# Optimization experiments

Measured on AMD Instinct MI355X. Metric: run time of the kernel, lower is better.

Reference implementation:

```python
import jax, jax.numpy as jnp
import numpy as np

M_MAX = 8
GN_GROUPS = 8  # _pick_gn_groups(64)
HEADS = 4
G_C = 19
PER_C = 16


def silu(x):
    return x * jax.nn.sigmoid(x)


def layer_norm(x, g, b, eps=1e-5):
    mu = x.mean(-1, keepdims=True)
    var = ((x - mu) ** 2).mean(-1, keepdims=True)
    return (x - mu) * jax.lax.rsqrt(var + eps) * g + b


def group_norm(x, g, b, eps=1e-5):
    N, C, H, W = x.shape
    xr = x.reshape(N, GN_GROUPS, C // GN_GROUPS, H, W)
    mu = xr.mean((2, 3, 4), keepdims=True)
    var = ((xr - mu) ** 2).mean((2, 3, 4), keepdims=True)
    xn = ((xr - mu) * jax.lax.rsqrt(var + eps)).reshape(N, C, H, W)
    return xn * g[:, None, None] + b[:, None, None]


def conv1x1(x, w):  # x [N,C,H,W], w [O,C]
    return jnp.einsum('nchw,oc->nohw', x, w)


def dw3x3(x, w):  # depthwise 3x3, w [C,1,3,3]
    return jax.lax.conv_general_dilated(x, w, (1, 1), 'SAME', feature_group_count=x.shape[1], dimension_numbers=('NCHW', 'OIHW', 'NCHW'))


def forward(board, stem_w, stem_g, stem_b, qw, qb, kw, kb, vw, vb, ow, ob, ln_g, ln_b, dw_w, gn1_g, gn1_b, pw_w, gn2_g, gn2_b, pol_w, pol_b, vh_w1, vh_b1, vh_w2, vh_b2, om_w, om_b, op_w1, op_b1, op_w2, op_b2):
    B, Cin, H, W = board.shape
    hid = stem_w.shape[0]
    hd = hid // HEADS
    g = board[:, :G_C]
    p = board[:, G_C:G_C + M_MAX * PER_C].reshape(B, M_MAX, PER_C, H, W)
    player_in = jnp.concatenate([jnp.broadcast_to(g[:, None], (B, M_MAX, G_C, H, W)), p], axis=2)
    x = conv1x1(player_in.reshape(B * M_MAX, G_C + PER_C, H, W), stem_w)
    x = silu(group_norm(x, stem_g, stem_b)).reshape(B, M_MAX, hid, H, W)
    m_each = jnp.argmax(board[:, 7:14, 0, 0], axis=1) + 2  # number of players in [2,8]
    present = jnp.arange(M_MAX) < m_each[:, None]  # [B, M_MAX] bool
    neg = jnp.finfo(board.dtype).min
    L = qw.shape[0]
    for i in range(L):
        tokens = x.transpose(0, 3, 4, 1, 2).reshape(B, H * W, M_MAX, hid)
        q = (tokens @ qw[i].T + qb[i]).reshape(B, H * W, M_MAX, HEADS, hd)
        k = (tokens @ kw[i].T + kb[i]).reshape(B, H * W, M_MAX, HEADS, hd)
        v = (tokens @ vw[i].T + vb[i]).reshape(B, H * W, M_MAX, HEADS, hd)
        logits = jnp.einsum('bnqhd,bnkhd->bnhqk', q, k) * (hd ** -0.5)
        logits = jnp.where(present[:, None, None, None, :], logits, neg)
        attn = jax.nn.softmax(logits, axis=-1)
        ao = jnp.einsum('bnhqk,bnkhd->bnqhd', attn, v).reshape(B, H * W, M_MAX, hid)
        tokens = layer_norm(tokens + ao @ ow[i].T + ob[i], ln_g[i], ln_b[i])
        xc = tokens.reshape(B, H, W, M_MAX, hid).transpose(0, 3, 4, 1, 2).reshape(B * M_MAX, hid, H, W)
        y = silu(group_norm(dw3x3(xc, dw_w[i]), gn1_g[i], gn1_b[i]))
        y = group_norm(conv1x1(y, pw_w[i]), gn2_g[i], gn2_b[i])
        xc = silu(xc + y)
        x = xc.reshape(B, M_MAX, hid, H, W) * present[:, :, None, None, None].astype(xc.dtype)
    x0 = x[:, 0]
    logits_p = (conv1x1(x0, pol_w) + pol_b[:, None, None]).reshape(B, H * W)
    pooled0 = x0.mean((2, 3))
    value = (silu(pooled0 @ vh_w1.T + vh_b1) @ vh_w2.T + vh_b2)[:, 0]
    move_all = (conv1x1(x.reshape(B * M_MAX, hid, H, W), om_w) + om_b[:, None, None]).reshape(B, M_MAX, M_MAX, H * W)
    pooled_all = x.mean((3, 4))
    param_all = (silu(pooled_all @ op_w1.T + op_b1) @ op_w2.T + op_b2).reshape(B, M_MAX, M_MAX, 5)
    idx = jnp.arange(M_MAX)
    pf = present[..., None]
    opp_move = move_all[:, idx, idx, :] * pf.astype(move_all.dtype)
    opp_param = param_all[:, idx, idx, :] * pf.astype(param_all.dtype)
    return (logits_p, value, opp_move, opp_param)


def setup_inputs() -> dict:
    key = jax.random.key(0)
    ks = iter(jax.random.split(key, 48))
    def rn(shape, s=0.1):
        return jax.random.normal(next(ks), shape, jnp.float32) * s
    B, H, W, C, L = 16, 32, 32, 64, 6
    inp = {
        'board': jax.random.normal(next(ks), (B, 149, H, W), jnp.float32),
        'stem_w': rn((C, 35)), 'stem_g': jnp.ones((C,)), 'stem_b': jnp.zeros((C,)),
        'qw': rn((L, C, C)), 'qb': rn((L, C), 0.01),
        'kw': rn((L, C, C)), 'kb': rn((L, C), 0.01),
        'vw': rn((L, C, C)), 'vb': rn((L, C), 0.01),
        'ow': rn((L, C, C)), 'ob': rn((L, C), 0.01),
        'ln_g': jnp.ones((L, C)), 'ln_b': jnp.zeros((L, C)),
        'dw_w': rn((L, C, 1, 3, 3)),
        'gn1_g': jnp.ones((L, C)), 'gn1_b': jnp.zeros((L, C)),
        'pw_w': rn((L, C, C)),
        'gn2_g': jnp.ones((L, C)), 'gn2_b': jnp.zeros((L, C)),
        'pol_w': rn((1, C)), 'pol_b': jnp.zeros((1,)),
        'vh_w1': rn((C, C)), 'vh_b1': jnp.zeros((C,)),
        'vh_w2': rn((1, C)), 'vh_b2': jnp.zeros((1,)),
        'om_w': rn((M_MAX, C)), 'om_b': jnp.zeros((M_MAX,)),
        'op_w1': rn((C, C)), 'op_b1': jnp.zeros((C,)),
        'op_w2': rn((M_MAX * 5, C)), 'op_b2': jnp.zeros((M_MAX * 5,)),
    }
    return inp


def reference(board, stem_w, stem_g, stem_b, qw, qb, kw, kb, vw, vb, ow, ob, ln_g, ln_b, dw_w, gn1_g, gn1_b, pw_w, gn2_g, gn2_b, pol_w, pol_b, vh_w1, vh_b1, vh_w2, vh_b2, om_w, om_b, op_w1, op_b1, op_w2, op_b2):
    return forward(board, stem_w, stem_g, stem_b, qw, qb, kw, kb, vw, vb, ow, ob, ln_g, ln_b, dw_w, gn1_g, gn1_b, pw_w, gn2_g, gn2_b, pol_w, pol_b, vh_w1, vh_b1, vh_w2, vh_b2, om_w, om_b, op_w1, op_b1, op_w2, op_b2)
```

## Files before the change

kernel.cpp:

```cpp
#include <hip/hip_runtime.h>
#include <cstddef>


#define WSX   0u
#define WST   8388608u
#define WSY   16777216u
#define WSS   25165824u
#define WSP   (WSS + 26624u)
#define WSPL  (WSP + 128u)

#define ATTN_LDS_BYTES ((4 * 64 * 64 + 8 * 64 * 8) * 4)

__device__ __forceinline__ float silu_f(float x) { return x / (1.f + __expf(-x)); }

__device__ __forceinline__ float wsum64(float v) {
#pragma unroll
  for (int s = 1; s < 64; s <<= 1) v += __shfl_xor(v, s);
  return v;
}

__device__ __forceinline__ float rowsum16(float v) {
  v += __int_as_float(__builtin_amdgcn_update_dpp(0, __float_as_int(v), 0x128, 0xf, 0xf, true));
  v += __int_as_float(__builtin_amdgcn_update_dpp(0, __float_as_int(v), 0x124, 0xf, 0xf, true));
  v += __int_as_float(__builtin_amdgcn_update_dpp(0, __float_as_int(v), 0x122, 0xf, 0xf, true));
  v += __int_as_float(__builtin_amdgcn_update_dpp(0, __float_as_int(v), 0x121, 0xf, 0xf, true));
  return v;
}

__device__ __forceinline__ float wsum64b(float v) {
  v = rowsum16(v);
  v += __shfl_xor(v, 16);
  v += __shfl_xor(v, 32);
  return v;
}

__global__ __launch_bounds__(256) void k_init(const float* __restrict__ board,
                                              float* __restrict__ ws) {
  int tid = threadIdx.x;
  for (unsigned i = blockIdx.x * 256 + tid; i < 26624u; i += 64u * 256u) ws[WSS + i] = 0.f;
  if (blockIdx.x == 0 && tid < 128) {
    int b = tid >> 3, m = tid & 7;
    float best = board[(size_t)(b * 149 + 7) * 1024];
    int bi = 0;
    for (int ch = 1; ch < 7; ++ch) {
      float v = board[(size_t)(b * 149 + 7 + ch) * 1024];
      if (v > best) { best = v; bi = ch; }
    }
    int m_each = bi + 2;
    ws[WSP + tid] = (m < m_each) ? 1.f : 0.f;
  }
}

__global__ __launch_bounds__(256) void k_stem(const float* __restrict__ board,
                                              const float* __restrict__ stem_w,
                                              float* __restrict__ ws) {
  __shared__ float A[147 * 64];
  __shared__ float WT[35 * 64];
  __shared__ float red_s[256], red_ss[256];
  int tid = threadIdx.x;
  int b = blockIdx.x >> 4, n0 = (blockIdx.x & 15) * 64;
  for (int i = tid; i < 147 * 64; i += 256) {
    int c = i >> 6, p = i & 63;
    A[i] = board[(size_t)(b * 149 + c) * 1024 + n0 + p];
  }
  for (int i = tid; i < 35 * 64; i += 256) {
    int o = i / 35, c = i % 35;
    WT[c * 64 + o] = stem_w[i];
  }
  __syncthreads();
  int o = tid & 63, wv = tid >> 6;
  float* X = ws + WSX;
  float st_s[8], st_ss[8];
#pragma unroll
  for (int m = 0; m < 8; ++m) { st_s[m] = 0.f; st_ss[m] = 0.f; }
  for (int m = 0; m < 8; ++m) {
    for (int k = 0; k < 4; ++k) {
      int q = wv + 4 * k;
      float a0 = 0.f, a1 = 0.f, a2 = 0.f, a3 = 0.f;
#pragma unroll
      for (int c = 0; c < 19; ++c) {
        float w = WT[c * 64 + o];
        float4 av = *(const float4*)&A[c * 64 + q * 4];
        a0 += av.x * w; a1 += av.y * w; a2 += av.z * w; a3 += av.w * w;
      }
#pragma unroll
      for (int j = 0; j < 16; ++j) {
        float w = WT[(19 + j) * 64 + o];
        float4 av = *(const float4*)&A[(19 + m * 16 + j) * 64 + q * 4];
        a0 += av.x * w; a1 += av.y * w; a2 += av.z * w; a3 += av.w * w;
      }
      int n = n0 + q * 4;
      float vals[4] = {a0, a1, a2, a3};
#pragma unroll
      for (int j = 0; j < 4; ++j) {
        X[((size_t)(b * 1024 + n + j) * 8 + m) * 64 + o] = vals[j];
        st_s[m] += vals[j];
        st_ss[m] += vals[j] * vals[j];
      }
    }
  }
  float* stats = ws + WSS;
  for (int m = 0; m < 8; ++m) {
    __syncthreads();
    red_s[tid] = st_s[m];
    red_ss[tid] = st_ss[m];
    __syncthreads();
    if (tid < 8) {
      float a = 0.f, a2 = 0.f;
      for (int w4 = 0; w4 < 4; ++w4)
        for (int j = 0; j < 8; ++j) {
          int t2 = w4 * 64 + tid * 8 + j;
          a += red_s[t2]; a2 += red_ss[t2];
        }
      atomicAdd(&stats[((b * 8 + m) * 8 + tid) * 2 + 0], a);
      atomicAdd(&stats[((b * 8 + m) * 8 + tid) * 2 + 1], a2);
    }
  }
}

__global__ __launch_bounds__(256) void k_gn_silu(float* __restrict__ X,
                                                 const float* __restrict__ g,
                                                 const float* __restrict__ bt,
                                                 const float* __restrict__ stats) {
  for (size_t idx = (size_t)blockIdx.x * 256 + threadIdx.x; idx < 8388608ull;
       idx += (size_t)2048 * 256) {
    int c = (int)(idx & 63);
    int m = (int)((idx >> 6) & 7);
    int b = (int)(idx >> 19);
    int gi = ((b * 8 + m) * 8 + (c >> 3)) * 2;
    float s = stats[gi], s2 = stats[gi + 1];
    float mean = s * (1.f / 8192.f);
    float var = s2 * (1.f / 8192.f) - mean * mean;
    float rstd = rsqrtf(var + 1e-5f);
    float v = (X[idx] - mean) * rstd * g[c] + bt[c];
    X[idx] = silu_f(v);
  }
}

#define FMA8(acc, WW)                                                      \
  acc[0] += t0.x * (WW); acc[1] += t0.y * (WW); acc[2] += t0.z * (WW);     \
  acc[3] += t0.w * (WW); acc[4] += t1.x * (WW); acc[5] += t1.y * (WW);     \
  acc[6] += t1.z * (WW); acc[7] += t1.w * (WW);

__global__ __launch_bounds__(512, 4) void k_attn(
    const float* __restrict__ Xin, const float* __restrict__ Yin,
    const float* __restrict__ s2p, const float* __restrict__ g2p,
    const float* __restrict__ b2p, float* __restrict__ T,
    const float* __restrict__ qw, const float* __restrict__ qb,
    const float* __restrict__ kw, const float* __restrict__ kb,
    const float* __restrict__ vw, const float* __restrict__ vb,
    const float* __restrict__ ow, const float* __restrict__ ob,
    const float* __restrict__ lng, const float* __restrict__ lnb,
    const float* __restrict__ present, int fused) {
  extern __shared__ float sm[];
  float* Wq = sm;
  float* Wk = sm + 4096;
  float* Wv = sm + 8192;
  float* Wo = sm + 12288;
  float* BUF = sm + 16384;
  int tid = threadIdx.x;
  int lane = tid & 63, wv = tid >> 6;
  int b = blockIdx.x >> 5;
  int n0 = (blockIdx.x & 31) * 32;
  for (int i = tid; i < 4096; i += 512) {
    int o = i >> 6, c = i & 63;
    Wq[c * 64 + o] = qw[i];
    Wk[c * 64 + o] = kw[i];
    Wv[c * 64 + o] = vw[i];
    Wo[c * 64 + o] = ow[i];
  }
  float bq = qb[lane], bk = kb[lane], bv = vb[lane], bo = ob[lane];
  float gl = lng[lane], bl = lnb[lane];
  unsigned pmask = 0;
#pragma unroll
  for (int m = 0; m < 8; ++m) pmask |= (present[b * 8 + m] > 0.5f) ? (1u << m) : 0u;
  float Ag[8], Bg[8];
  if (fused) {
    int g = lane >> 3;
    float gw = g2p[lane], bw_ = b2p[lane];
#pragma unroll
    for (int m = 0; m < 8; ++m) {
      int gi = ((b * 8 + m) * 8 + g) * 2;
      float sg = s2p[gi], sg2 = s2p[gi + 1];
      float mean = sg * (1.f / 8192.f);
      float var = sg2 * (1.f / 8192.f) - mean * mean;
      float rstd = rsqrtf(var + 1e-5f);
      Ag[m] = rstd * gw;
      Bg[m] = bw_ - mean * Ag[m];
    }
  }
  __syncthreads();
  float* bw = BUF + wv * 512;
  const int sw = lane & 12;
  for (int j = 0; j < 4; ++j) {
    int n = n0 + wv * 4 + j;
    size_t pbase = ((size_t)(b * 1024 + n) * 8) * 64 + lane;
    float tok[8];
    if (fused) {
#pragma unroll
      for (int m = 0; m < 8; ++m) {
        float tv = Xin[pbase + m * 64];
        float yv = Yin[pbase + m * 64];
        float z = tv + (yv * Ag[m] + Bg[m]);
        float pres = ((pmask >> m) & 1) ? 1.f : 0.f;
        tok[m] = silu_f(z) * pres;
      }
    } else {
#pragma unroll
      for (int m = 0; m < 8; ++m) tok[m] = Xin[pbase + m * 64];
    }
    *(float4*)&bw[(lane * 8) ^ sw]     = make_float4(tok[0], tok[1], tok[2], tok[3]);
    *(float4*)&bw[(lane * 8 + 4) ^ sw] = make_float4(tok[4], tok[5], tok[6], tok[7]);
    __asm__ volatile("" ::: "memory");
    float aq[8], ak[8], av[8];
#pragma unroll
    for (int m = 0; m < 8; ++m) { aq[m] = bq; ak[m] = bk; av[m] = bv; }
#pragma unroll
    for (int c = 0; c < 64; ++c) {
      float4 t0 = *(const float4*)&bw[(c * 8) ^ (c & 12)];
      float4 t1 = *(const float4*)&bw[(c * 8 + 4) ^ (c & 12)];
      float wq_ = Wq[c * 64 + lane];
      float wk_ = Wk[c * 64 + lane];
      float wv_ = Wv[c * 64 + lane];
      FMA8(aq, wq_)
      FMA8(ak, wk_)
      FMA8(av, wv_)
    }
    float ao[8];
#pragma unroll
    for (int mq = 0; mq < 8; ++mq) {
      float lg[8];
#pragma unroll
      for (int mk = 0; mk < 8; ++mk)
        lg[mk] = rowsum16(aq[mq] * ak[mk]) * 0.25f;
      float mx = -3.0e38f;
#pragma unroll
      for (int mk = 0; mk < 8; ++mk)
        if ((pmask >> mk) & 1) mx = fmaxf(mx, lg[mk]);
      float se = 0.f, acc = 0.f;
#pragma unroll
      for (int mk = 0; mk < 8; ++mk) {
        float e = ((pmask >> mk) & 1) ? __expf(lg[mk] - mx) : 0.f;
        se += e;
        acc += e * av[mk];
      }
      ao[mq] = acc * __builtin_amdgcn_rcpf(se);
    }
    __asm__ volatile("" ::: "memory");
    *(float4*)&bw[(lane * 8) ^ sw]     = make_float4(ao[0], ao[1], ao[2], ao[3]);
    *(float4*)&bw[(lane * 8 + 4) ^ sw] = make_float4(ao[4], ao[5], ao[6], ao[7]);
    __asm__ volatile("" ::: "memory");
    float z[8];
#pragma unroll
    for (int m = 0; m < 8; ++m) z[m] = bo;
#pragma unroll
    for (int c = 0; c < 64; ++c) {
      float4 t0 = *(const float4*)&bw[(c * 8) ^ (c & 12)];
      float4 t1 = *(const float4*)&bw[(c * 8 + 4) ^ (c & 12)];
      float wo_ = Wo[c * 64 + lane];
      FMA8(z, wo_)
    }
    __asm__ volatile("" ::: "memory");
    float* tp = T + pbase;
#pragma unroll
    for (int m = 0; m < 8; ++m) {
      float r = tok[m] + z[m];
      float mean = wsum64b(r) * (1.f / 64.f);
      float d = r - mean;
      float var = wsum64b(d * d) * (1.f / 64.f);
      float rstd = rsqrtf(var + 1e-5f);
      tp[m * 64] = d * rstd * gl + bl;
    }
  }
}

__global__ __launch_bounds__(256) void k_dw(const float* __restrict__ T, float* __restrict__ Y,
                                            const float* __restrict__ dww,
                                            float* __restrict__ stats) {
  __shared__ float red_s[256], red_ss[256];
  int tid = threadIdx.x;
  int b = blockIdx.x >> 5, r = blockIdx.x & 31;
  int half = tid >> 7;
  int mc4 = tid & 127;
  int m = mc4 >> 4, c4 = mc4 & 15, c0 = c4 * 4;
  float4 w9[9];
#pragma unroll
  for (int t = 0; t < 9; ++t) {
    w9[t].x = dww[(c0 + 0) * 9 + t];
    w9[t].y = dww[(c0 + 1) * 9 + t];
    w9[t].z = dww[(c0 + 2) * 9 + t];
    w9[t].w = dww[(c0 + 3) * 9 + t];
  }
  float s = 0.f, ss = 0.f;
  const size_t plane = (size_t)b * 524288 + (size_t)m * 64 + c0;
  for (int ci = 0; ci < 16; ++ci) {
    int col = half * 16 + ci;
    float4 acc = make_float4(0.f, 0.f, 0.f, 0.f);
#pragma unroll
    for (int dh = -1; dh <= 1; ++dh) {
      int rr = r + dh;
      if (rr < 0 || rr > 31) continue;
#pragma unroll
      for (int dx = -1; dx <= 1; ++dx) {
        int cc = col + dx;
        if (cc < 0 || cc > 31) continue;
        float4 tv = *(const float4*)&T[plane + (size_t)(rr * 32 + cc) * 512];
        float4 w = w9[(dh + 1) * 3 + dx + 1];
        acc.x += tv.x * w.x; acc.y += tv.y * w.y;
        acc.z += tv.z * w.z; acc.w += tv.w * w.w;
      }
    }
    *(float4*)&Y[plane + (size_t)(r * 32 + col) * 512] = acc;
    s += acc.x + acc.y + acc.z + acc.w;
    ss += acc.x * acc.x + acc.y * acc.y + acc.z * acc.z + acc.w * acc.w;
  }
  red_s[tid] = s;
  red_ss[tid] = ss;
  __syncthreads();
  if (tid < 64) {
    int mm = tid >> 3, g = tid & 7;
    float a = 0.f, a2 = 0.f;
#pragma unroll
    for (int hh = 0; hh < 2; ++hh)
#pragma unroll
      for (int e = 0; e < 2; ++e) {
        int idx = hh * 128 + mm * 16 + g * 2 + e;
        a += red_s[idx];
        a2 += red_ss[idx];
      }
    atomicAdd(&stats[((b * 8 + mm) * 8 + g) * 2 + 0], a);
    atomicAdd(&stats[((b * 8 + mm) * 8 + g) * 2 + 1], a2);
  }
}

__global__ __launch_bounds__(256) void k_pw(float* __restrict__ Y, const float* __restrict__ pw,
                                            const float* __restrict__ g1,
                                            const float* __restrict__ b1,
                                            const float* __restrict__ s1,
                                            float* __restrict__ s2) {
  __shared__ float PWT[4096];
  __shared__ float HB[4][256];
  __shared__ float red_s[256], red_ss[256];
  int tid = threadIdx.x, lane = tid & 63, wv = tid >> 6;
  int bm = blockIdx.x >> 2, pt = blockIdx.x & 3;
  int b = bm >> 3, m = bm & 7;
  int n0 = pt * 256;
  for (int i = tid; i < 4096; i += 256) {
    int o = i >> 6, c = i & 63;
    PWT[c * 64 + o] = pw[i];
  }
  int g = lane >> 3;
  float sg = s1[(bm * 8 + g) * 2], sg2 = s1[(bm * 8 + g) * 2 + 1];
  float mean = sg * (1.f / 8192.f);
  float var = sg2 * (1.f / 8192.f) - mean * mean;
  float rstd = rsqrtf(var + 1e-5f);
  float A = rstd * g1[lane];
  float Bc = b1[lane] - mean * A;
  __syncthreads();
  float st = 0.f, st2 = 0.f;
  const size_t base = (size_t)b * 1024 * 512 + (size_t)m * 64 + lane;
  for (int it = 0; it < 16; ++it) {
    int n = n0 + it * 16 + wv * 4;
    float h[4];
#pragma unroll
    for (int jj = 0; jj < 4; ++jj) {
      float y = Y[base + (size_t)(n + jj) * 512];
      h[jj] = silu_f(y * A + Bc);
    }
    *(float4*)&HB[wv][lane * 4] = make_float4(h[0], h[1], h[2], h[3]);
    __asm__ volatile("" ::: "memory");
    float a0 = 0.f, a1 = 0.f, a2 = 0.f, a3 = 0.f;
#pragma unroll 8
    for (int c = 0; c < 64; ++c) {
      float4 hh = *(const float4*)&HB[wv][c * 4];
      float w = PWT[c * 64 + lane];
      a0 += hh.x * w; a1 += hh.y * w; a2 += hh.z * w; a3 += hh.w * w;
    }
    float vals[4] = {a0, a1, a2, a3};
#pragma unroll
    for (int jj = 0; jj < 4; ++jj) {
      Y[base + (size_t)(n + jj) * 512] = vals[jj];
      st += vals[jj];
      st2 += vals[jj] * vals[jj];
    }
    __asm__ volatile("" ::: "memory");
  }
  red_s[tid] = st;
  red_ss[tid] = st2;
  __syncthreads();
  if (tid < 8) {
    float a = 0.f, a2 = 0.f;
    for (int w4 = 0; w4 < 4; ++w4)
      for (int j = 0; j < 8; ++j) {
        int t2 = w4 * 64 + tid * 8 + j;
        a += red_s[t2]; a2 += red_ss[t2];
      }
    atomicAdd(&s2[(bm * 8 + tid) * 2 + 0], a);
    atomicAdd(&s2[(bm * 8 + tid) * 2 + 1], a2);
  }
}

__global__ __launch_bounds__(256) void k_fuse(const float* __restrict__ T,
                                              const float* __restrict__ Y,
                                              float* __restrict__ X,
                                              const float* __restrict__ g2,
                                              const float* __restrict__ b2,
                                              const float* __restrict__ s2,
                                              const float* __restrict__ present) {
  int tid = threadIdx.x, lane = tid & 63, wv = tid >> 6;
  int bm = blockIdx.x >> 3, pt = blockIdx.x & 7;
  int b = bm >> 3, m = bm & 7;
  int g = lane >> 3;
  float sg = s2[(bm * 8 + g) * 2], sg2 = s2[(bm * 8 + g) * 2 + 1];
  float mean = sg * (1.f / 8192.f);
  float var = sg2 * (1.f / 8192.f) - mean * mean;
  float rstd = rsqrtf(var + 1e-5f);
  float A = rstd * g2[lane];
  float Bc = b2[lane] - mean * A;
  float pres = present[bm];
  const size_t base = (size_t)b * 1024 * 512 + (size_t)m * 64 + lane;
  int n0 = pt * 128;
  for (int i2 = 0; i2 < 32; ++i2) {
    int n = n0 + i2 * 4 + wv;
    size_t idx = base + (size_t)n * 512;
    float z = T[idx] + (Y[idx] * A + Bc);
    X[idx] = silu_f(z) * pres;
  }
}

__global__ __launch_bounds__(256) void k_heads_px(const float* __restrict__ X,
                                                  const float* __restrict__ pol_w,
                                                  const float* __restrict__ pol_b,
                                                  const float* __restrict__ om_w,
                                                  const float* __restrict__ om_b,
                                                  const float* __restrict__ present,
                                                  float* __restrict__ out) {
  int tid = threadIdx.x, lane = tid & 63, wv = tid >> 6;
  int b = blockIdx.x >> 4, n0 = (blockIdx.x & 15) * 64;
  float pw_ = pol_w[lane];
  for (int it = 0; it < 16; ++it) {
    int n = n0 + wv * 16 + it;
    const float* xp = X + ((size_t)(b * 1024 + n) * 8) * 64 + lane;
#pragma unroll
    for (int m = 0; m < 8; ++m) {
      float v = xp[m * 64];
      float d = wsum64(v * om_w[m * 64 + lane]);
      if (m == 0) {
        float dp = wsum64(v * pw_);
        if (lane == 0) out[b * 1024 + n] = dp + pol_b[0];
      }
      if (lane == 0)
        out[16400u + (size_t)(b * 8 + m) * 1024 + n] = (d + om_b[m]) * present[b * 8 + m];
    }
  }
}

__global__ __launch_bounds__(256) void k_pool(const float* __restrict__ X,
                                              float* __restrict__ pooled) {
  __shared__ float red[256];
  int tid = threadIdx.x, lane = tid & 63, wv = tid >> 6;
  int b = blockIdx.x >> 3, m = blockIdx.x & 7;
  float s = 0.f;
  for (int p = wv; p < 1024; p += 4)
    s += X[((size_t)(b * 1024 + p) * 8 + m) * 64 + lane];
  red[tid] = s;
  __syncthreads();
  if (tid < 64)
    pooled[(b * 8 + m) * 64 + tid] =
        (red[tid] + red[tid + 64] + red[tid + 128] + red[tid + 192]) * (1.f / 1024.f);
}

__global__ __launch_bounds__(64) void k_heads_vec(
    const float* __restrict__ pooled, const float* __restrict__ vh_w1,
    const float* __restrict__ vh_b1, const float* __restrict__ vh_w2,
    const float* __restrict__ vh_b2, const float* __restrict__ op_w1,
    const float* __restrict__ op_b1, const float* __restrict__ op_w2,
    const float* __restrict__ op_b2, const float* __restrict__ present,
    float* __restrict__ out) {
  int lane = threadIdx.x;
  int b = blockIdx.x >> 3, m = blockIdx.x & 7;
  const float* pp = pooled + (b * 8 + m) * 64;
  float h = op_b1[lane];
  for (int c = 0; c < 64; ++c) h += pp[c] * op_w1[lane * 64 + c];
  h = silu_f(h);
  float pres = present[b * 8 + m];
  for (int jj = 0; jj < 5; ++jj) {
    float d = wsum64(h * op_w2[(m * 5 + jj) * 64 + lane]);
    if (lane == 0) out[147472u + (b * 8 + m) * 5 + jj] = (d + op_b2[m * 5 + jj]) * pres;
  }
  if (m == 0) {
    float hv = vh_b1[lane];
    for (int c = 0; c < 64; ++c) hv += pp[c] * vh_w1[lane * 64 + c];
    hv = silu_f(hv);
    float dv = wsum64(hv * vh_w2[lane]);
    if (lane == 0) out[16384u + b] = dv + vh_b2[0];
  }
}

extern "C" void kernel_launch(void* const* d_in, const int* in_sizes, int n_in,
                              void* d_out, int out_size, void* d_ws, size_t ws_size,
                              hipStream_t stream) {
  const float* board  = (const float*)d_in[0];
  const float* stem_w = (const float*)d_in[1];
  const float* stem_g = (const float*)d_in[2];
  const float* stem_b = (const float*)d_in[3];
  const float* qw = (const float*)d_in[4];
  const float* qb = (const float*)d_in[5];
  const float* kw = (const float*)d_in[6];
  const float* kb = (const float*)d_in[7];
  const float* vw = (const float*)d_in[8];
  const float* vb = (const float*)d_in[9];
  const float* ow = (const float*)d_in[10];
  const float* ob = (const float*)d_in[11];
  const float* ln_g = (const float*)d_in[12];
  const float* ln_b = (const float*)d_in[13];
  const float* dw_w = (const float*)d_in[14];
  const float* gn1_g = (const float*)d_in[15];
  const float* gn1_b = (const float*)d_in[16];
  const float* pw_w = (const float*)d_in[17];
  const float* gn2_g = (const float*)d_in[18];
  const float* gn2_b = (const float*)d_in[19];
  const float* pol_w = (const float*)d_in[20];
  const float* pol_b = (const float*)d_in[21];
  const float* vh_w1 = (const float*)d_in[22];
  const float* vh_b1 = (const float*)d_in[23];
  const float* vh_w2 = (const float*)d_in[24];
  const float* vh_b2 = (const float*)d_in[25];
  const float* om_w = (const float*)d_in[26];
  const float* om_b = (const float*)d_in[27];
  const float* op_w1 = (const float*)d_in[28];
  const float* op_b1 = (const float*)d_in[29];
  const float* op_w2 = (const float*)d_in[30];
  const float* op_b2 = (const float*)d_in[31];
  float* ws = (float*)d_ws;
  float* out = (float*)d_out;

  (void)hipFuncSetAttribute((const void*)k_attn,
                            hipFuncAttributeMaxDynamicSharedMemorySize,
                            ATTN_LDS_BYTES);

  k_init<<<64, 256, 0, stream>>>(board, ws);
  k_stem<<<256, 256, 0, stream>>>(board, stem_w, ws);
  k_gn_silu<<<2048, 256, 0, stream>>>(ws + WSX, stem_g, stem_b, ws + WSS);

  for (int i = 0; i < 6; ++i) {
    float* s1 = ws + WSS + (size_t)(1 + 2 * i) * 2048;
    float* s2 = ws + WSS + (size_t)(2 + 2 * i) * 2048;
    if (i == 0) {
      k_attn<<<512, 512, ATTN_LDS_BYTES, stream>>>(
          ws + WSX, ws + WSX, ws + WSS, gn2_g, gn2_b, ws + WST,
          qw, qb, kw, kb, vw, vb, ow, ob, ln_g, ln_b, ws + WSP, 0);
    } else {
      float* s2prev = ws + WSS + (size_t)(2 * i) * 2048;
      k_attn<<<512, 512, ATTN_LDS_BYTES, stream>>>(
          ws + WST, ws + WSY, s2prev, gn2_g + (i - 1) * 64, gn2_b + (i - 1) * 64,
          ws + WST, qw + i * 4096, qb + i * 64, kw + i * 4096, kb + i * 64,
          vw + i * 4096, vb + i * 64, ow + i * 4096, ob + i * 64, ln_g + i * 64,
          ln_b + i * 64, ws + WSP, 1);
    }
    k_dw<<<512, 256, 0, stream>>>(ws + WST, ws + WSY, dw_w + i * 576, s1);
    k_pw<<<512, 256, 0, stream>>>(ws + WSY, pw_w + i * 4096, gn1_g + i * 64,
                                  gn1_b + i * 64, s1, s2);
  }
  k_fuse<<<1024, 256, 0, stream>>>(ws + WST, ws + WSY, ws + WSX, gn2_g + 5 * 64,
                                   gn2_b + 5 * 64, ws + WSS + (size_t)12 * 2048,
                                   ws + WSP);

  k_heads_px<<<256, 256, 0, stream>>>(ws + WSX, pol_w, pol_b, om_w, om_b, ws + WSP, out);
  k_pool<<<128, 256, 0, stream>>>(ws + WSX, ws + WSPL);
  k_heads_vec<<<128, 64, 0, stream>>>(ws + WSPL, vh_w1, vh_b1, vh_w2, vh_b2, op_w1,
                                      op_b1, op_w2, op_b2, ws + WSP, out);
}
```

Measured before the change: 1.411 ms.

## Skip absent-player work in attention, depthwise and pointwise layers

Stores each board's player count in the workspace. The attention kernel is templated on a compile-time player bound (4, 6 or 8) chosen per block, so projections, softmax and output only cover slots that can be present. The depthwise conv threads and pointwise blocks for absent players now skip their work entirely, which removes padded computation and memory traffic. The cost is that buffers and GroupNorm stats for absent slots keep stale or zero values, so correctness depends on downstream masking; three template instantiations also grow code size.

```diff
diff --git a/kernel.cpp b/kernel.cpp
--- a/kernel.cpp
+++ b/kernel.cpp
@@ -7,7 +7,7 @@
 #define WSY   16777216u
 #define WSS   25165824u
 #define WSP   (WSS + 26624u)
-#define WSPL  (WSP + 128u)
+#define WSPL  (WSP + 160u)
 
 #define ATTN_LDS_BYTES ((4 * 64 * 64 + 8 * 64 * 8) * 4)
 
@@ -48,6 +48,7 @@
     }
     int m_each = bi + 2;
     ws[WSP + tid] = (m < m_each) ? 1.f : 0.f;
+    if (m == 0) ws[WSP + 128 + b] = (float)m_each;
   }
 }
 
@@ -137,10 +138,100 @@
   }
 }
 
-#define FMA8(acc, WW)                                                      \
-  acc[0] += t0.x * (WW); acc[1] += t0.y * (WW); acc[2] += t0.z * (WW);     \
-  acc[3] += t0.w * (WW); acc[4] += t1.x * (WW); acc[5] += t1.y * (WW);     \
-  acc[6] += t1.z * (WW); acc[7] += t1.w * (WW);
+template <int MB>
+__device__ __forceinline__ void attn_core(
+    const float* __restrict__ Xin, const float* __restrict__ Yin,
+    float* __restrict__ T, const float* Wq, const float* Wk, const float* Wv,
+    const float* Wo, float* bw, int b, int n0, int wv, int lane, int sw,
+    float bq, float bk, float bv, float bo, float gl, float bl,
+    unsigned pmask, const float* Ag, const float* Bg, int fused) {
+  for (int j = 0; j < 4; ++j) {
+    int n = n0 + wv * 4 + j;
+    size_t pbase = ((size_t)(b * 1024 + n) * 8) * 64 + lane;
+    float tok[8] = {0.f, 0.f, 0.f, 0.f, 0.f, 0.f, 0.f, 0.f};
+    if (fused) {
+#pragma unroll
+      for (int m = 0; m < MB; ++m) {
+        float tv = Xin[pbase + m * 64];
+        float yv = Yin[pbase + m * 64];
+        float z = tv + (yv * Ag[m] + Bg[m]);
+        float pres = ((pmask >> m) & 1) ? 1.f : 0.f;
+        tok[m] = silu_f(z) * pres;
+      }
+    } else {
+#pragma unroll
+      for (int m = 0; m < MB; ++m) tok[m] = Xin[pbase + m * 64];
+    }
+    *(float4*)&bw[(lane * 8) ^ sw]     = make_float4(tok[0], tok[1], tok[2], tok[3]);
+    *(float4*)&bw[(lane * 8 + 4) ^ sw] = make_float4(tok[4], tok[5], tok[6], tok[7]);
+    __asm__ volatile("" ::: "memory");
+    float aq[MB], ak[MB], av[MB];
+#pragma unroll
+    for (int m = 0; m < MB; ++m) { aq[m] = bq; ak[m] = bk; av[m] = bv; }
+#pragma unroll
+    for (int c = 0; c < 64; ++c) {
+      float4 t0 = *(const float4*)&bw[(c * 8) ^ (c & 12)];
+      float4 t1 = *(const float4*)&bw[(c * 8 + 4) ^ (c & 12)];
+      float tarr[8] = {t0.x, t0.y, t0.z, t0.w, t1.x, t1.y, t1.z, t1.w};
+      float wq_ = Wq[c * 64 + lane];
+      float wk_ = Wk[c * 64 + lane];
+      float wv_ = Wv[c * 64 + lane];
+#pragma unroll
+      for (int m = 0; m < MB; ++m) {
+        aq[m] = fmaf(tarr[m], wq_, aq[m]);
+        ak[m] = fmaf(tarr[m], wk_, ak[m]);
+        av[m] = fmaf(tarr[m], wv_, av[m]);
+      }
+    }
+    float ao[8] = {0.f, 0.f, 0.f, 0.f, 0.f, 0.f, 0.f, 0.f};
+#pragma unroll
+    for (int mq = 0; mq < MB; ++mq) {
+      float lg[MB];
+#pragma unroll
+      for (int mk = 0; mk < MB; ++mk)
+        lg[mk] = rowsum16(aq[mq] * ak[mk]) * 0.25f;
+      float mx = -3.0e38f;
+#pragma unroll
+      for (int mk = 0; mk < MB; ++mk)
+        if ((pmask >> mk) & 1) mx = fmaxf(mx, lg[mk]);
+      float se = 0.f, acc = 0.f;
+#pragma unroll
+      for (int mk = 0; mk < MB; ++mk) {
+        float e = ((pmask >> mk) & 1) ? __expf(lg[mk] - mx) : 0.f;
+        se += e;
+        acc += e * av[mk];
+      }
+      ao[mq] = acc * __builtin_amdgcn_rcpf(se);
+    }
+    __asm__ volatile("" ::: "memory");
+    *(float4*)&bw[(lane * 8) ^ sw]     = make_float4(ao[0], ao[1], ao[2], ao[3]);
+    *(float4*)&bw[(lane * 8 + 4) ^ sw] = make_float4(ao[4], ao[5], ao[6], ao[7]);
+    __asm__ volatile("" ::: "memory");
+    float z[MB];
+#pragma unroll
+    for (int m = 0; m < MB; ++m) z[m] = bo;
+#pragma unroll
+    for (int c = 0; c < 64; ++c) {
+      float4 t0 = *(const float4*)&bw[(c * 8) ^ (c & 12)];
+      float4 t1 = *(const float4*)&bw[(c * 8 + 4) ^ (c & 12)];
+      float tarr[8] = {t0.x, t0.y, t0.z, t0.w, t1.x, t1.y, t1.z, t1.w};
+      float wo_ = Wo[c * 64 + lane];
+#pragma unroll
+      for (int m = 0; m < MB; ++m) z[m] = fmaf(tarr[m], wo_, z[m]);
+    }
+    __asm__ volatile("" ::: "memory");
+    float* tp = T + pbase;
+#pragma unroll
+    for (int m = 0; m < MB; ++m) {
+      float r = tok[m] + z[m];
+      float mean = wsum64b(r) * (1.f / 64.f);
+      float d = r - mean;
+      float var = wsum64b(d * d) * (1.f / 64.f);
+      float rstd = rsqrtf(var + 1e-5f);
+      tp[m * 64] = d * rstd * gl + bl;
+    }
+  }
+}
 
 __global__ __launch_bounds__(512, 4) void k_attn(
     const float* __restrict__ Xin, const float* __restrict__ Yin,
@@ -174,6 +265,7 @@
   unsigned pmask = 0;
 #pragma unroll
   for (int m = 0; m < 8; ++m) pmask |= (present[b * 8 + m] > 0.5f) ? (1u << m) : 0u;
+  int mea = (int)present[128 + b];
   float Ag[8], Bg[8];
   if (fused) {
     int g = lane >> 3;
@@ -192,127 +284,60 @@
   __syncthreads();
   float* bw = BUF + wv * 512;
   const int sw = lane & 12;
-  for (int j = 0; j < 4; ++j) {
-    int n = n0 + wv * 4 + j;
-    size_t pbase = ((size_t)(b * 1024 + n) * 8) * 64 + lane;
-    float tok[8];
-    if (fused) {
-#pragma unroll
-      for (int m = 0; m < 8; ++m) {
-        float tv = Xin[pbase + m * 64];
-        float yv = Yin[pbase + m * 64];
-        float z = tv + (yv * Ag[m] + Bg[m]);
-        float pres = ((pmask >> m) & 1) ? 1.f : 0.f;
-        tok[m] = silu_f(z) * pres;
-      }
-    } else {
-#pragma unroll
-      for (int m = 0; m < 8; ++m) tok[m] = Xin[pbase + m * 64];
-    }
-    *(float4*)&bw[(lane * 8) ^ sw]     = make_float4(tok[0], tok[1], tok[2], tok[3]);
-    *(float4*)&bw[(lane * 8 + 4) ^ sw] = make_float4(tok[4], tok[5], tok[6], tok[7]);
-    __asm__ volatile("" ::: "memory");
-    float aq[8], ak[8], av[8];
-#pragma unroll
-    for (int m = 0; m < 8; ++m) { aq[m] = bq; ak[m] = bk; av[m] = bv; }
-#pragma unroll
-    for (int c = 0; c < 64; ++c) {
-      float4 t0 = *(const float4*)&bw[(c * 8) ^ (c & 12)];
-      float4 t1 = *(const float4*)&bw[(c * 8 + 4) ^ (c & 12)];
-      float wq_ = Wq[c * 64 + lane];
-      float wk_ = Wk[c * 64 + lane];
-      float wv_ = Wv[c * 64 + lane];
-      FMA8(aq, wq_)
-      FMA8(ak, wk_)
-      FMA8(av, wv_)
-    }
-    float ao[8];
-#pragma unroll
-    for (int mq = 0; mq < 8; ++mq) {
-      float lg[8];
-#pragma unroll
-      for (int mk = 0; mk < 8; ++mk)
-        lg[mk] = rowsum16(aq[mq] * ak[mk]) * 0.25f;
-      float mx = -3.0e38f;
-#pragma unroll
-      for (int mk = 0; mk < 8; ++mk)
-        if ((pmask >> mk) & 1) mx = fmaxf(mx, lg[mk]);
-      float se = 0.f, acc = 0.f;
-#pragma unroll
-      for (int mk = 0; mk < 8; ++mk) {
-        float e = ((pmask >> mk) & 1) ? __expf(lg[mk] - mx) : 0.f;
-        se += e;
-        acc += e * av[mk];
-      }
-      ao[mq] = acc * __builtin_amdgcn_rcpf(se);
-    }
-    __asm__ volatile("" ::: "memory");
-    *(float4*)&bw[(lane * 8) ^ sw]     = make_float4(ao[0], ao[1], ao[2], ao[3]);
-    *(float4*)&bw[(lane * 8 + 4) ^ sw] = make_float4(ao[4], ao[5], ao[6], ao[7]);
-    __asm__ volatile("" ::: "memory");
-    float z[8];
-#pragma unroll
-    for (int m = 0; m < 8; ++m) z[m] = bo;
-#pragma unroll
-    for (int c = 0; c < 64; ++c) {
-      float4 t0 = *(const float4*)&bw[(c * 8) ^ (c & 12)];
-      float4 t1 = *(const float4*)&bw[(c * 8 + 4) ^ (c & 12)];
-      float wo_ = Wo[c * 64 + lane];
-      FMA8(z, wo_)
-    }
-    __asm__ volatile("" ::: "memory");
-    float* tp = T + pbase;
-#pragma unroll
-    for (int m = 0; m < 8; ++m) {
-      float r = tok[m] + z[m];
-      float mean = wsum64b(r) * (1.f / 64.f);
-      float d = r - mean;
-      float var = wsum64b(d * d) * (1.f / 64.f);
-      float rstd = rsqrtf(var + 1e-5f);
-      tp[m * 64] = d * rstd * gl + bl;
-    }
-  }
+  if (mea <= 4)
+    attn_core<4>(Xin, Yin, T, Wq, Wk, Wv, Wo, bw, b, n0, wv, lane, sw,
+                 bq, bk, bv, bo, gl, bl, pmask, Ag, Bg, fused);
+  else if (mea <= 6)
+    attn_core<6>(Xin, Yin, T, Wq, Wk, Wv, Wo, bw, b, n0, wv, lane, sw,
+                 bq, bk, bv, bo, gl, bl, pmask, Ag, Bg, fused);
+  else
+    attn_core<8>(Xin, Yin, T, Wq, Wk, Wv, Wo, bw, b, n0, wv, lane, sw,
+                 bq, bk, bv, bo, gl, bl, pmask, Ag, Bg, fused);
 }
 
 __global__ __launch_bounds__(256) void k_dw(const float* __restrict__ T, float* __restrict__ Y,
                                             const float* __restrict__ dww,
-                                            float* __restrict__ stats) {
+                                            float* __restrict__ stats,
+                                            const float* __restrict__ present) {
   __shared__ float red_s[256], red_ss[256];
   int tid = threadIdx.x;
   int b = blockIdx.x >> 5, r = blockIdx.x & 31;
   int half = tid >> 7;
   int mc4 = tid & 127;
   int m = mc4 >> 4, c4 = mc4 & 15, c0 = c4 * 4;
-  float4 w9[9];
-#pragma unroll
-  for (int t = 0; t < 9; ++t) {
-    w9[t].x = dww[(c0 + 0) * 9 + t];
-    w9[t].y = dww[(c0 + 1) * 9 + t];
-    w9[t].z = dww[(c0 + 2) * 9 + t];
-    w9[t].w = dww[(c0 + 3) * 9 + t];
-  }
+  int mea = (int)present[128 + b];
   float s = 0.f, ss = 0.f;
-  const size_t plane = (size_t)b * 524288 + (size_t)m * 64 + c0;
-  for (int ci = 0; ci < 16; ++ci) {
-    int col = half * 16 + ci;
-    float4 acc = make_float4(0.f, 0.f, 0.f, 0.f);
-#pragma unroll
-    for (int dh = -1; dh <= 1; ++dh) {
-      int rr = r + dh;
-      if (rr < 0 || rr > 31) continue;
-#pragma unroll
-      for (int dx = -1; dx <= 1; ++dx) {
-        int cc = col + dx;
-        if (cc < 0 || cc > 31) continue;
-        float4 tv = *(const float4*)&T[plane + (size_t)(rr * 32 + cc) * 512];
-        float4 w = w9[(dh + 1) * 3 + dx + 1];
-        acc.x += tv.x * w.x; acc.y += tv.y * w.y;
-        acc.z += tv.z * w.z; acc.w += tv.w * w.w;
-      }
-    }
-    *(float4*)&Y[plane + (size_t)(r * 32 + col) * 512] = acc;
-    s += acc.x + acc.y + acc.z + acc.w;
-    ss += acc.x * acc.x + acc.y * acc.y + acc.z * acc.z + acc.w * acc.w;
+  if (m < mea) {
+    float4 w9[9];
+#pragma unroll
+    for (int t = 0; t < 9; ++t) {
+      w9[t].x = dww[(c0 + 0) * 9 + t];
+      w9[t].y = dww[(c0 + 1) * 9 + t];
+      w9[t].z = dww[(c0 + 2) * 9 + t];
+      w9[t].w = dww[(c0 + 3) * 9 + t];
+    }
+    const size_t plane = (size_t)b * 524288 + (size_t)m * 64 + c0;
+    for (int ci = 0; ci < 16; ++ci) {
+      int col = half * 16 + ci;
+      float4 acc = make_float4(0.f, 0.f, 0.f, 0.f);
+#pragma unroll
+      for (int dh = -1; dh <= 1; ++dh) {
+        int rr = r + dh;
+        if (rr < 0 || rr > 31) continue;
+#pragma unroll
+        for (int dx = -1; dx <= 1; ++dx) {
+          int cc = col + dx;
+          if (cc < 0 || cc > 31) continue;
+          float4 tv = *(const float4*)&T[plane + (size_t)(rr * 32 + cc) * 512];
+          float4 w = w9[(dh + 1) * 3 + dx + 1];
+          acc.x += tv.x * w.x; acc.y += tv.y * w.y;
+          acc.z += tv.z * w.z; acc.w += tv.w * w.w;
+        }
+      }
+      *(float4*)&Y[plane + (size_t)(r * 32 + col) * 512] = acc;
+      s += acc.x + acc.y + acc.z + acc.w;
+      ss += acc.x * acc.x + acc.y * acc.y + acc.z * acc.z + acc.w * acc.w;
+    }
   }
   red_s[tid] = s;
   red_ss[tid] = ss;
@@ -337,13 +362,15 @@
                                             const float* __restrict__ g1,
                                             const float* __restrict__ b1,
                                             const float* __restrict__ s1,
-                                            float* __restrict__ s2) {
+                                            float* __restrict__ s2,
+                                            const float* __restrict__ present) {
   __shared__ float PWT[4096];
   __shared__ float HB[4][256];
   __shared__ float red_s[256], red_ss[256];
   int tid = threadIdx.x, lane = tid & 63, wv = tid >> 6;
   int bm = blockIdx.x >> 2, pt = blockIdx.x & 3;
   int b = bm >> 3, m = bm & 7;
+  if (m >= (int)present[128 + b]) return;
   int n0 = pt * 256;
   for (int i = tid; i < 4096; i += 256) {
     int o = i >> 6, c = i & 63;
@@ -558,9 +585,9 @@
           vw + i * 4096, vb + i * 64, ow + i * 4096, ob + i * 64, ln_g + i * 64,
           ln_b + i * 64, ws + WSP, 1);
     }
-    k_dw<<<512, 256, 0, stream>>>(ws + WST, ws + WSY, dw_w + i * 576, s1);
+    k_dw<<<512, 256, 0, stream>>>(ws + WST, ws + WSY, dw_w + i * 576, s1, ws + WSP);
     k_pw<<<512, 256, 0, stream>>>(ws + WSY, pw_w + i * 4096, gn1_g + i * 64,
-                                  gn1_b + i * 64, s1, s2);
+                                  gn1_b + i * 64, s1, s2, ws + WSP);
   }
   k_fuse<<<1024, 256, 0, stream>>>(ws + WST, ws + WSY, ws + WSX, gn2_g + 5 * 64,
                                    gn2_b + 5 * 64, ws + WSS + (size_t)12 * 2048,
```

After: 1.265 ms. 1.12x faster.
